# Kernel tuning notes

Measured on AMD Instinct MI355X. Metric: run time of the kernel, lower is better.

Reference implementation:

```python
import jax, jax.numpy as jnp
import numpy as np

N, E, D_IN, D_H, G = 50000, 800000, 300, 128, 128


def gat_conv(x, src, dst, W, att_src, att_dst, bias):
    # PyG GATConv, heads=1, concat, negative_slope=0.2, self-loops already appended.
    h = x @ W                              # [N, F]
    a_s = h @ att_src                      # [N]
    a_d = h @ att_dst                      # [N]
    e = jax.nn.leaky_relu(a_s[src] + a_d[dst], 0.2)   # [E+N]
    m = jax.ops.segment_max(e, dst, num_segments=h.shape[0])
    ex = jnp.exp(e - m[dst])
    denom = jax.ops.segment_sum(ex, dst, num_segments=h.shape[0])
    alpha = ex / denom[dst]                # softmax over in-edges of each dst
    out = jax.ops.segment_sum(alpha[:, None] * h[src], dst, num_segments=h.shape[0])
    return out + bias


def setup_inputs() -> dict:
    key = jax.random.key(0)
    ks = jax.random.split(key, 12)
    x = jax.random.normal(ks[0], (N, D_IN), dtype=jnp.float32)
    edge_index = jax.random.randint(ks[1], (2, E), 0, N)
    batch = jnp.sort(jax.random.randint(ks[2], (N,), 0, G))
    pos = jax.random.randint(ks[3], (N,), 0, 2).astype(bool)
    s = 0.05
    W1 = jax.random.normal(ks[4], (D_IN, D_H), dtype=jnp.float32) * s
    as1 = jax.random.normal(ks[5], (D_H,), dtype=jnp.float32) * s
    ad1 = jax.random.normal(ks[6], (D_H,), dtype=jnp.float32) * s
    b1 = jnp.zeros((D_H,), dtype=jnp.float32)
    W2 = jax.random.normal(ks[7], (D_H, D_H), dtype=jnp.float32) * s
    as2 = jax.random.normal(ks[8], (D_H,), dtype=jnp.float32) * s
    ad2 = jax.random.normal(ks[9], (D_H,), dtype=jnp.float32) * s
    b2 = jnp.zeros((D_H,), dtype=jnp.float32)
    Wfc = jax.random.normal(ks[10], (D_H, 1), dtype=jnp.float32) * s
    bfc = jnp.zeros((1,), dtype=jnp.float32)
    return {"x": x, "edge_index": edge_index, "batch": batch, "pos": pos,
            "num_graphs": G, "W1": W1, "as1": as1, "ad1": ad1, "b1": b1,
            "W2": W2, "as2": as2, "ad2": ad2, "b2": b2, "Wfc": Wfc, "bfc": bfc}


def reference(x, edge_index, batch, pos, num_graphs, W1, as1, ad1, b1,
              W2, as2, ad2, b2, Wfc, bfc):
    n = x.shape[0]
    loop = jnp.arange(n)
    src = jnp.concatenate([edge_index[0], loop])
    dst = jnp.concatenate([edge_index[1], loop])
    h = gat_conv(x, src, dst, W1, as1, ad1, b1)
    h = jax.nn.gelu(h, approximate=False)
    # dropout is identity in eval mode
    h = gat_conv(h, src, dst, W2, as2, ad2, b2)   # [N, 128]
    # masked per-graph mean: logits[g] = mean over nodes with batch==g and pos
    w = pos.astype(h.dtype)                       # [N]
    sums = jax.ops.segment_sum(h * w[:, None], batch, num_segments=num_graphs)
    cnt = jax.ops.segment_sum(w, batch, num_segments=num_graphs)
    logits = sums / jnp.maximum(cnt, 1.0)[:, None]          # [G, 128]
    scores = (jax.nn.gelu(logits, approximate=False) @ Wfc + bfc).reshape(-1, num_graphs)
    return scores, logits
```

## Files before the change

### kernel.cpp

```cpp
#include <hip/hip_runtime.h>
#include <math.h>

#define NN 50000
#define EE 800000
#define DIN 300
#define DH 128
#define NG 128
#define RSIZE 6250

typedef __attribute__((ext_vector_type(8))) short short8;
typedef __attribute__((ext_vector_type(4))) float floatx4;

__device__ __forceinline__ float gelu_exact(float x) {
  return 0.5f * x * (1.0f + erff(x * 0.7071067811865476f));
}

__device__ __forceinline__ void split_bf16(float v, unsigned short& hi, unsigned short& lo) {
  unsigned int u = __float_as_uint(v);
  hi = (unsigned short)(u >> 16);
  float fh = __uint_as_float((unsigned int)hi << 16);
  lo = (unsigned short)(__float_as_uint(v - fh) >> 16);
}

__device__ __forceinline__ unsigned short f2bf_rne(float x) {
  unsigned int u = __float_as_uint(x);
  unsigned int r = (u + 0x7FFFu + ((u >> 16) & 1u)) >> 16;
  return (unsigned short)r;
}

__device__ __forceinline__ float bf_lo(unsigned u) { return __uint_as_float(u << 16); }
__device__ __forceinline__ float bf_hi(unsigned u) { return __uint_as_float(u & 0xFFFF0000u); }

__device__ __forceinline__ void async_ld16(void* lds, const void* g) {
  __builtin_amdgcn_global_load_lds(
      (const __attribute__((address_space(1))) unsigned int*)(unsigned long long)g,
      (__attribute__((address_space(3))) unsigned int*)(unsigned int)(unsigned long long)lds,
      16, 0, 0);
}


__global__ __launch_bounds__(256) void count_part_kernel(const int* __restrict__ ei,
                                                         int* __restrict__ deg,
                                                         int blocksPerRange) {
  const int r = blockIdx.x & 7;
  const int t = blockIdx.x >> 3;
  const int lo = r * RSIZE, hi = lo + RSIZE;
  const int total = EE + NN;
  const int step = blocksPerRange * 256;
  for (int e0 = t * 256; e0 < total; e0 += step) {
    int e = e0 + threadIdx.x;
    if (e < total) {
      int d = (e < EE) ? ei[EE + e] : (e - EE);
      if (d >= lo && d < hi) atomicAdd(&deg[d], 1);
    }
  }
}

__global__ __launch_bounds__(1024) void scan_part_kernel(const int* __restrict__ deg,
                                                         int* __restrict__ rowptr,
                                                         int* __restrict__ bsum) {
  __shared__ int wsum[16];
  const int tid = threadIdx.x;
  const int lane = tid & 63;
  const int wid = tid >> 6;
  int idx = blockIdx.x * 1024 + tid;
  int v = (idx < NN) ? deg[idx] : 0;
  int x = v;
#pragma unroll
  for (int d = 1; d < 64; d <<= 1) {
    int y = __shfl_up(x, d, 64);
    if (lane >= d) x += y;
  }
  if (lane == 63) wsum[wid] = x;
  __syncthreads();
  if (wid == 0) {
    int s = (lane < 16) ? wsum[lane] : 0;
#pragma unroll
    for (int d = 1; d < 16; d <<= 1) {
      int y = __shfl_up(s, d, 64);
      if (lane >= d) s += y;
    }
    if (lane < 16) wsum[lane] = s;
  }
  __syncthreads();
  int woff = (wid > 0) ? wsum[wid - 1] : 0;
  int incl = x + woff;
  if (idx < NN) rowptr[idx] = incl - v;
  if (tid == 1023) bsum[blockIdx.x] = incl;
}

__global__ __launch_bounds__(64) void scan_sums_kernel(const int* __restrict__ bsum,
                                                       int* __restrict__ boff, int nb) {
  int lane = threadIdx.x;
  int v = (lane < nb) ? bsum[lane] : 0;
  int x = v;
#pragma unroll
  for (int d = 1; d < 64; d <<= 1) {
    int y = __shfl_up(x, d, 64);
    if (lane >= d) x += y;
  }
  if (lane < nb) boff[lane] = x - v;
  if (lane == nb - 1) boff[nb] = x;
}

__global__ __launch_bounds__(256) void scan_add_kernel(int* __restrict__ rowptr,
                                                       const int* __restrict__ boff,
                                                       int* __restrict__ cursor, int nb) {
  int i = blockIdx.x * 256 + threadIdx.x;
  if (i < NN) {
    int r = rowptr[i] + boff[i >> 10];
    rowptr[i] = r;
    cursor[i] = r;
  } else if (i == NN) {
    rowptr[NN] = boff[nb];
  }
}

__global__ __launch_bounds__(256) void scatter_part_kernel(const int* __restrict__ ei,
                                                           int* __restrict__ cursor,
                                                           int* __restrict__ colA,
                                                           int blocksPerRange) {
  const int r = blockIdx.x & 7;
  const int t = blockIdx.x >> 3;
  const int lo = r * RSIZE, hi = lo + RSIZE;
  const int total = EE + NN;
  const int step = blocksPerRange * 256;
  for (int e0 = t * 256; e0 < total; e0 += step) {
    int e = e0 + threadIdx.x;
    if (e < total) {
      int d = (e < EE) ? ei[EE + e] : (e - EE);
      if (d >= lo && d < hi) {
        int s = (e < EE) ? ei[e] : d;
        int p = atomicAdd(&cursor[d], 1);
        colA[p] = s;
      }
    }
  }
}


__global__ __launch_bounds__(256) void convert_bt_kernel(const float* __restrict__ B,
                                                         unsigned short* __restrict__ Bth,
                                                         unsigned short* __restrict__ Btl,
                                                         int K, int Kpad) {
  int i = blockIdx.x * 256 + threadIdx.x;
  int n = i / Kpad, k = i % Kpad;
  if (n >= 128) return;
  float v = (k < K) ? B[(long)k * 128 + n] : 0.f;
  unsigned short h, l;
  split_bf16(v, h, l);
  Bth[(long)n * Kpad + k] = h;
  Btl[(long)n * Kpad + k] = l;
}


__global__ __launch_bounds__(256) void gemm_mfma_kernel(
    const float* __restrict__ A,
    const unsigned short* __restrict__ Bth, const unsigned short* __restrict__ Btl,
    unsigned short* __restrict__ C, int M, int K, int Kpad,
    const float* __restrict__ avs, const float* __restrict__ avd,
    float* __restrict__ aS, float* __restrict__ aD) {
  __shared__ __align__(16) unsigned short Bls[2][2][128 * 32];

  const int tid = threadIdx.x;
  const int lane = tid & 63;
  const int w = tid >> 6;
  const int wr = w & 1;
  const int wc = w >> 1;
  const int q = lane >> 4;
  const int m16 = lane & 15;
  const int row0 = blockIdx.x * 32;
  const int myrow = row0 + wr * 16 + m16;
  const bool rok = myrow < M;
  const long abase = (long)myrow * K;

  const int rl = lane >> 2, qq0 = lane & 3;
  const int nb0 = w * 16 + rl;
  const int nb1 = 64 + w * 16 + rl;
  const long boff0 = (long)nb0 * Kpad + (long)((qq0 ^ ((nb0 >> 1) & 3)) * 8);
  const long boff1 = (long)nb1 * Kpad + (long)((qq0 ^ ((nb1 >> 1) & 3)) * 8);

  floatx4 acc[4];
#pragma unroll
  for (int i = 0; i < 4; i++) acc[i] = (floatx4)(0.f);

  const int nsteps = Kpad / 32;

  float4 vA0, vA1, nA0, nA1;
  nA0 = nA1 = make_float4(0.f, 0.f, 0.f, 0.f);

  auto stageB = [&](int s, int nb) {
    const int k0 = s * 32;
    async_ld16(&Bls[nb][0][(w * 16) * 32], Bth + boff0 + k0);
    async_ld16(&Bls[nb][0][(64 + w * 16) * 32], Bth + boff1 + k0);
    async_ld16(&Bls[nb][1][(w * 16) * 32], Btl + boff0 + k0);
    async_ld16(&Bls[nb][1][(64 + w * 16) * 32], Btl + boff1 + k0);
  };
  auto loadA = [&](int s, float4& x0, float4& x1) {
    const int k0 = s * 32 + q * 8;
    x0 = make_float4(0.f, 0.f, 0.f, 0.f);
    x1 = x0;
    if (rok) {
      if (k0 + 4 <= K) x0 = *(const float4*)&A[abase + k0];
      if (k0 + 8 <= K) x1 = *(const float4*)&A[abase + k0 + 4];
    }
  };

  stageB(0, 0);
  loadA(0, vA0, vA1);
  __syncthreads();

  for (int s = 0; s < nsteps; s++) {
    const int cur = s & 1;
    if (s + 1 < nsteps) {
      stageB(s + 1, 1 ^ cur);
      loadA(s + 1, nA0, nA1);
    }
    float av[8] = {vA0.x, vA0.y, vA0.z, vA0.w, vA1.x, vA1.y, vA1.z, vA1.w};
    union {
      unsigned u[4];
      short8 s8;
    } Uh, Ul;
#pragma unroll
    for (int i = 0; i < 4; i++) {
      unsigned short ha, la, hb, lb;
      split_bf16(av[2 * i], ha, la);
      split_bf16(av[2 * i + 1], hb, lb);
      Uh.u[i] = (unsigned)ha | ((unsigned)hb << 16);
      Ul.u[i] = (unsigned)la | ((unsigned)lb << 16);
    }
    short8 afh = Uh.s8, afl = Ul.s8;
#pragma unroll
    for (int ct = 0; ct < 4; ct++) {
      int n = wc * 64 + ct * 16 + m16;
      int qv = (q ^ ((n >> 1) & 3)) * 8;
      short8 bfh = *(const short8*)&Bls[cur][0][n * 32 + qv];
      short8 bfl = *(const short8*)&Bls[cur][1][n * 32 + qv];
      acc[ct] = __builtin_amdgcn_mfma_f32_16x16x32_bf16(afh, bfh, acc[ct], 0, 0, 0);
      acc[ct] = __builtin_amdgcn_mfma_f32_16x16x32_bf16(afh, bfl, acc[ct], 0, 0, 0);
      acc[ct] = __builtin_amdgcn_mfma_f32_16x16x32_bf16(afl, bfh, acc[ct], 0, 0, 0);
    }
    vA0 = nA0;
    vA1 = nA1;
    __syncthreads();
  }

  float avs_r[4], avd_r[4];
#pragma unroll
  for (int ct = 0; ct < 4; ct++) {
    avs_r[ct] = avs[wc * 64 + ct * 16 + m16];
    avd_r[ct] = avd[wc * 64 + ct * 16 + m16];
  }
  float psA[4], pdA[4];
#pragma unroll
  for (int reg = 0; reg < 4; reg++) {
    int grow = row0 + wr * 16 + q * 4 + reg;
    bool ok = grow < M;
    float ps = 0.f, pd = 0.f;
#pragma unroll
    for (int ct = 0; ct < 4; ct++) {
      float c = acc[ct][reg];
      if (ok) C[(long)grow * 128 + wc * 64 + ct * 16 + m16] = f2bf_rne(c);
      ps = fmaf(c, avs_r[ct], ps);
      pd = fmaf(c, avd_r[ct], pd);
    }
#pragma unroll
    for (int d = 1; d < 16; d <<= 1) {
      ps += __shfl_xor(ps, d, 64);
      pd += __shfl_xor(pd, d, 64);
    }
    psA[reg] = ps;
    pdA[reg] = pd;
  }
  float* redS = (float*)&Bls[0][0][0];
  float* redD = redS + 32;
  if (wc == 1 && m16 == 0) {
#pragma unroll
    for (int reg = 0; reg < 4; reg++) {
      int rloc = wr * 16 + q * 4 + reg;
      redS[rloc] = psA[reg];
      redD[rloc] = pdA[reg];
    }
  }
  __syncthreads();
  if (wc == 0 && m16 == 0) {
#pragma unroll
    for (int reg = 0; reg < 4; reg++) {
      int rloc = wr * 16 + q * 4 + reg;
      int grow = row0 + rloc;
      if (grow < M) {
        aS[grow] = psA[reg] + redS[rloc];
        aD[grow] = pdA[reg] + redD[rloc];
      }
    }
  }
}


__global__ __launch_bounds__(256) void aggregate_kernel(const int* __restrict__ rowptr,
                                                        const int* __restrict__ colA,
                                                        const float* __restrict__ aS,
                                                        const float* __restrict__ aD,
                                                        const unsigned short* __restrict__ Hb,
                                                        const float* __restrict__ bias,
                                                        float* __restrict__ out,
                                                        int apply_gelu) {
  const int lane = threadIdx.x & 63;
  const int dst = blockIdx.x * 4 + (threadIdx.x >> 6);
  if (dst >= NN) return;
  const int start = rowptr[dst];
  const int end = rowptr[dst + 1];
  const int deg = end - start;
  const float ad = aD[dst];
  const int half = lane >> 5;
  const int fl = lane & 31;

  float a0 = 0.f, a1 = 0.f, a2 = 0.f, a3 = 0.f;

  if (deg <= 64) {
    int src = 0;
    float e = -__builtin_inff();
    if (lane < deg) {
      src = colA[start + lane];
      float v = aS[src] + ad;
      e = (v > 0.f) ? v : 0.2f * v;
    }
    float mx = e;
#pragma unroll
    for (int d = 1; d < 64; d <<= 1) mx = fmaxf(mx, __shfl_xor(mx, d, 64));
    float ew = (lane < deg) ? expf(e - mx) : 0.f;
    float ss = ew;
#pragma unroll
    for (int d = 1; d < 64; d <<= 1) ss += __shfl_xor(ss, d, 64);
    float wgt = ew * (1.f / ss);
    for (int j = 0; j < deg; j += 8) {
      int sj[4];
      float wj[4];
#pragma unroll
      for (int i = 0; i < 4; i++) {
        int idx = j + 2 * i + half;
        sj[i] = __shfl(src, idx & 63, 64);
        float ww = __shfl(wgt, idx & 63, 64);
        wj[i] = (idx < deg) ? ww : 0.f;
      }
      uint2 u[4];
#pragma unroll
      for (int i = 0; i < 4; i++) u[i] = *(const uint2*)&Hb[(long)sj[i] * DH + fl * 4];
#pragma unroll
      for (int i = 0; i < 4; i++) {
        a0 = fmaf(wj[i], bf_lo(u[i].x), a0);
        a1 = fmaf(wj[i], bf_hi(u[i].x), a1);
        a2 = fmaf(wj[i], bf_lo(u[i].y), a2);
        a3 = fmaf(wj[i], bf_hi(u[i].y), a3);
      }
    }
  } else {
    float m = -__builtin_inff(), ssum = 0.f;
    for (int c0 = start; c0 < end; c0 += 64) {
      int i = c0 + lane;
      float e = -__builtin_inff();
      if (i < end) {
        int s = colA[i];
        float v = aS[s] + ad;
        e = (v > 0.f) ? v : 0.2f * v;
      }
      float cm = e;
#pragma unroll
      for (int d = 1; d < 64; d <<= 1) cm = fmaxf(cm, __shfl_xor(cm, d, 64));
      float ce = (i < end) ? expf(e - cm) : 0.f;
      float cs = ce;
#pragma unroll
      for (int d = 1; d < 64; d <<= 1) cs += __shfl_xor(cs, d, 64);
      float nm = fmaxf(m, cm);
      ssum = ssum * expf(m - nm) + cs * expf(cm - nm);
      m = nm;
    }
    float inv = 1.f / ssum;
    for (int c0 = start; c0 < end; c0 += 64) {
      int i = c0 + lane;
      int src = 0;
      float wgt = 0.f;
      if (i < end) {
        src = colA[i];
        float v = aS[src] + ad;
        float e = (v > 0.f) ? v : 0.2f * v;
        wgt = expf(e - m) * inv;
      }
      int lim = min(64, end - c0);
      for (int j = 0; j < lim; j += 4) {
        int j0 = j + half;
        int j1 = j + 2 + half;
        int sj0 = __shfl(src, j0 & 63, 64);
        float wj0 = __shfl(wgt, j0 & 63, 64);
        if (j0 >= lim) wj0 = 0.f;
        int sj1 = __shfl(src, j1 & 63, 64);
        float wj1 = __shfl(wgt, j1 & 63, 64);
        if (j1 >= lim) wj1 = 0.f;
        uint2 u0 = *(const uint2*)&Hb[(long)sj0 * DH + fl * 4];
        uint2 u1 = *(const uint2*)&Hb[(long)sj1 * DH + fl * 4];
        a0 = fmaf(wj0, bf_lo(u0.x), a0);
        a1 = fmaf(wj0, bf_hi(u0.x), a1);
        a2 = fmaf(wj0, bf_lo(u0.y), a2);
        a3 = fmaf(wj0, bf_hi(u0.y), a3);
        a0 = fmaf(wj1, bf_lo(u1.x), a0);
        a1 = fmaf(wj1, bf_hi(u1.x), a1);
        a2 = fmaf(wj1, bf_lo(u1.y), a2);
        a3 = fmaf(wj1, bf_hi(u1.y), a3);
      }
    }
  }

  a0 += __shfl_xor(a0, 32, 64);
  a1 += __shfl_xor(a1, 32, 64);
  a2 += __shfl_xor(a2, 32, 64);
  a3 += __shfl_xor(a3, 32, 64);

  if (half == 0) {
    float4 b = *(const float4*)&bias[fl * 4];
    float r0 = a0 + b.x;
    float r1 = a1 + b.y;
    float r2 = a2 + b.z;
    float r3 = a3 + b.w;
    if (apply_gelu) {
      r0 = gelu_exact(r0); r1 = gelu_exact(r1);
      r2 = gelu_exact(r2); r3 = gelu_exact(r3);
    }
    *(float4*)&out[(long)dst * DH + fl * 4] = make_float4(r0, r1, r2, r3);
  }
}


__global__ __launch_bounds__(128) void pool_kernel(const float* __restrict__ H,
                                                   const int* __restrict__ batch,
                                                   const int* __restrict__ pos,
                                                   float* __restrict__ sums,
                                                   float* __restrict__ cnt) {
  const int CH = 64;
  int n0 = blockIdx.x * CH;
  int n1 = min(n0 + CH, NN);
  int f = threadIdx.x;
  float acc = 0.f, c = 0.f;
  int g = batch[n0];
  for (int n = n0; n < n1; n++) {
    int gn = batch[n];
    if (gn != g) {
      atomicAdd(&sums[g * DH + f], acc);
      if (f == 0) atomicAdd(&cnt[g], c);
      acc = 0.f; c = 0.f; g = gn;
    }
    if (pos[n]) {
      acc += H[(long)n * DH + f];
      c += 1.f;
    }
  }
  atomicAdd(&sums[g * DH + f], acc);
  if (f == 0) atomicAdd(&cnt[g], c);
}


__global__ __launch_bounds__(128) void head_kernel(const float* __restrict__ sums,
                                                   const float* __restrict__ cnt,
                                                   const float* __restrict__ Wfc,
                                                   const float* __restrict__ bfc,
                                                   float* __restrict__ out) {
  int g = blockIdx.x;
  int f = threadIdx.x;
  float c = fmaxf(cnt[g], 1.f);
  float logit = sums[g * DH + f] / c;
  out[NG + g * DH + f] = logit;
  float gl = gelu_exact(logit) * Wfc[f];
  __shared__ float red[2];
#pragma unroll
  for (int d = 1; d < 64; d <<= 1) gl += __shfl_xor(gl, d, 64);
  int lane = f & 63, w = f >> 6;
  if (lane == 0) red[w] = gl;
  __syncthreads();
  if (f == 0) out[g] = red[0] + red[1] + bfc[0];
}


extern "C" void kernel_launch(void* const* d_in, const int* in_sizes, int n_in,
                              void* d_out, int out_size, void* d_ws, size_t ws_size,
                              hipStream_t stream) {
  const float* x   = (const float*)d_in[0];
  const int* ei    = (const int*)d_in[1];
  const int* batch = (const int*)d_in[2];
  const int* pos   = (const int*)d_in[3];
  const float* W1  = (const float*)d_in[5];
  const float* as1 = (const float*)d_in[6];
  const float* ad1 = (const float*)d_in[7];
  const float* b1  = (const float*)d_in[8];
  const float* W2  = (const float*)d_in[9];
  const float* as2 = (const float*)d_in[10];
  const float* ad2 = (const float*)d_in[11];
  const float* b2  = (const float*)d_in[12];
  const float* Wfc = (const float*)d_in[13];
  const float* bfc = (const float*)d_in[14];
  float* out = (float*)d_out;

  const int KP1 = 320;
  const int KP2 = 128;
  const int NB_SCAN = (NN + 1023) / 1024;
  const int BPR = 416;

  char* ws = (char*)d_ws;
  size_t off = 0;
  auto nxt = [&](size_t b) -> void* {
    size_t p = off;
    off += (b + 255) & ~(size_t)255;
    return (void*)(ws + p);
  };
  int* rowptr = (int*)nxt((NN + 1) * sizeof(int));
  int* cursor = (int*)nxt(NN * sizeof(int));
  int* colA   = (int*)nxt((size_t)(EE + NN) * sizeof(int));
  int* bsum   = (int*)nxt((NB_SCAN + 1) * sizeof(int));
  int* boff   = (int*)nxt((NB_SCAN + 1) * sizeof(int));
  float* aS   = (float*)nxt((size_t)2 * NN * sizeof(float));
  float* aD   = aS + NN;
  unsigned short* bufAb = (unsigned short*)nxt((size_t)NN * DH * sizeof(short));
  float* bufB = (float*)nxt((size_t)NN * DH * sizeof(float));
  float* sums = (float*)nxt((size_t)(NG * DH + NG) * sizeof(float));
  float* cnt  = sums + NG * DH;
  unsigned short* Bt1h = (unsigned short*)nxt((size_t)128 * KP1 * sizeof(short));
  unsigned short* Bt1l = (unsigned short*)nxt((size_t)128 * KP1 * sizeof(short));
  unsigned short* Bt2h = (unsigned short*)nxt((size_t)128 * KP2 * sizeof(short));
  unsigned short* Bt2l = (unsigned short*)nxt((size_t)128 * KP2 * sizeof(short));

  hipMemsetAsync(cursor, 0, NN * sizeof(int), stream);
  hipMemsetAsync(sums, 0, (NG * DH + NG) * sizeof(float), stream);

  convert_bt_kernel<<<(128 * KP1 + 255) / 256, 256, 0, stream>>>(W1, Bt1h, Bt1l, DIN, KP1);
  convert_bt_kernel<<<(128 * KP2 + 255) / 256, 256, 0, stream>>>(W2, Bt2h, Bt2l, DH, KP2);

  count_part_kernel<<<8 * BPR, 256, 0, stream>>>(ei, cursor, BPR);
  scan_part_kernel<<<NB_SCAN, 1024, 0, stream>>>(cursor, rowptr, bsum);
  scan_sums_kernel<<<1, 64, 0, stream>>>(bsum, boff, NB_SCAN);
  scan_add_kernel<<<(NN + 1 + 255) / 256, 256, 0, stream>>>(rowptr, boff, cursor, NB_SCAN);
  scatter_part_kernel<<<8 * BPR, 256, 0, stream>>>(ei, cursor, colA, BPR);

  const int gblocks = (NN + 31) / 32;
  gemm_mfma_kernel<<<gblocks, 256, 0, stream>>>(x, Bt1h, Bt1l, bufAb, NN, DIN, KP1,
                                                as1, ad1, aS, aD);
  aggregate_kernel<<<(NN + 3) / 4, 256, 0, stream>>>(rowptr, colA, aS, aD, bufAb, b1, bufB, 1);
  gemm_mfma_kernel<<<gblocks, 256, 0, stream>>>(bufB, Bt2h, Bt2l, bufAb, NN, DH, KP2,
                                                as2, ad2, aS, aD);
  aggregate_kernel<<<(NN + 3) / 4, 256, 0, stream>>>(rowptr, colA, aS, aD, bufAb, b2, bufB, 0);
  pool_kernel<<<(NN + 63) / 64, 128, 0, stream>>>(bufB, batch, pos, sums, cnt);
  head_kernel<<<NG, 128, 0, stream>>>(sums, cnt, Wfc, bfc, out);
}
```

Before: 348.4 us.

## Retile GEMM to 64x64 blocks over a 2D grid with atomic attention-score reduction

The GEMM block tile changes from 32 rows × 128 cols to 64 rows × 64 cols, with blockIdx.y choosing the column half. Each wave now owns 16 rows × 64 cols. This halves the shared B tile and removes the intra-block LDS reduction and barrier for the attention dot products. The per-row partial scores from the two column halves are now combined with float atomicAdd, which needs extra memsets of aS/aD before each GEMM. The trade-off is that each A row is read by two blocks instead of one, and the atomics make the summation order nondeterministic.

Result: no change. 355.0 us (+1.9%).

```diff
diff --git a/kernel.cpp b/kernel.cpp
--- a/kernel.cpp
+++ b/kernel.cpp
@@ -160,25 +160,22 @@
     unsigned short* __restrict__ C, int M, int K, int Kpad,
     const float* __restrict__ avs, const float* __restrict__ avd,
     float* __restrict__ aS, float* __restrict__ aD) {
-  __shared__ __align__(16) unsigned short Bls[2][2][128 * 32];
+  __shared__ __align__(16) unsigned short Bls[2][2][64 * 32];
 
   const int tid = threadIdx.x;
   const int lane = tid & 63;
   const int w = tid >> 6;
-  const int wr = w & 1;
-  const int wc = w >> 1;
   const int q = lane >> 4;
   const int m16 = lane & 15;
-  const int row0 = blockIdx.x * 32;
-  const int myrow = row0 + wr * 16 + m16;
+  const int row0 = blockIdx.x * 64 + w * 16;
+  const int col0 = blockIdx.y * 64;
+  const int myrow = row0 + m16;
   const bool rok = myrow < M;
   const long abase = (long)myrow * K;
 
   const int rl = lane >> 2, qq0 = lane & 3;
-  const int nb0 = w * 16 + rl;
-  const int nb1 = 64 + w * 16 + rl;
-  const long boff0 = (long)nb0 * Kpad + (long)((qq0 ^ ((nb0 >> 1) & 3)) * 8);
-  const long boff1 = (long)nb1 * Kpad + (long)((qq0 ^ ((nb1 >> 1) & 3)) * 8);
+  const int nl = w * 16 + rl;
+  const long boff = (long)(col0 + nl) * Kpad + (long)((qq0 ^ ((nl >> 1) & 3)) * 8);
 
   floatx4 acc[4];
 #pragma unroll
@@ -191,10 +188,8 @@
 
   auto stageB = [&](int s, int nb) {
     const int k0 = s * 32;
-    async_ld16(&Bls[nb][0][(w * 16) * 32], Bth + boff0 + k0);
-    async_ld16(&Bls[nb][0][(64 + w * 16) * 32], Bth + boff1 + k0);
-    async_ld16(&Bls[nb][1][(w * 16) * 32], Btl + boff0 + k0);
-    async_ld16(&Bls[nb][1][(64 + w * 16) * 32], Btl + boff1 + k0);
+    async_ld16(&Bls[nb][0][(w * 16) * 32], Bth + boff + k0);
+    async_ld16(&Bls[nb][1][(w * 16) * 32], Btl + boff + k0);
   };
   auto loadA = [&](int s, float4& x0, float4& x1) {
     const int k0 = s * 32 + q * 8;
@@ -232,7 +227,7 @@
     short8 afh = Uh.s8, afl = Ul.s8;
 #pragma unroll
     for (int ct = 0; ct < 4; ct++) {
-      int n = wc * 64 + ct * 16 + m16;
+      int n = ct * 16 + m16;
       int qv = (q ^ ((n >> 1) & 3)) * 8;
       short8 bfh = *(const short8*)&Bls[cur][0][n * 32 + qv];
       short8 bfl = *(const short8*)&Bls[cur][1][n * 32 + qv];
@@ -248,19 +243,18 @@
   float avs_r[4], avd_r[4];
 #pragma unroll
   for (int ct = 0; ct < 4; ct++) {
-    avs_r[ct] = avs[wc * 64 + ct * 16 + m16];
-    avd_r[ct] = avd[wc * 64 + ct * 16 + m16];
-  }
-  float psA[4], pdA[4];
+    avs_r[ct] = avs[col0 + ct * 16 + m16];
+    avd_r[ct] = avd[col0 + ct * 16 + m16];
+  }
 #pragma unroll
   for (int reg = 0; reg < 4; reg++) {
-    int grow = row0 + wr * 16 + q * 4 + reg;
+    int grow = row0 + q * 4 + reg;
     bool ok = grow < M;
     float ps = 0.f, pd = 0.f;
 #pragma unroll
     for (int ct = 0; ct < 4; ct++) {
       float c = acc[ct][reg];
-      if (ok) C[(long)grow * 128 + wc * 64 + ct * 16 + m16] = f2bf_rne(c);
+      if (ok) C[(long)grow * 128 + col0 + ct * 16 + m16] = f2bf_rne(c);
       ps = fmaf(c, avs_r[ct], ps);
       pd = fmaf(c, avd_r[ct], pd);
     }
@@ -269,29 +263,9 @@
       ps += __shfl_xor(ps, d, 64);
       pd += __shfl_xor(pd, d, 64);
     }
-    psA[reg] = ps;
-    pdA[reg] = pd;
-  }
-  float* redS = (float*)&Bls[0][0][0];
-  float* redD = redS + 32;
-  if (wc == 1 && m16 == 0) {
-#pragma unroll
-    for (int reg = 0; reg < 4; reg++) {
-      int rloc = wr * 16 + q * 4 + reg;
-      redS[rloc] = psA[reg];
-      redD[rloc] = pdA[reg];
-    }
-  }
-  __syncthreads();
-  if (wc == 0 && m16 == 0) {
-#pragma unroll
-    for (int reg = 0; reg < 4; reg++) {
-      int rloc = wr * 16 + q * 4 + reg;
-      int grow = row0 + rloc;
-      if (grow < M) {
-        aS[grow] = psA[reg] + redS[rloc];
-        aD[grow] = pdA[reg] + redD[rloc];
-      }
+    if (m16 == 0 && ok) {
+      atomicAdd(&aS[grow], ps);
+      atomicAdd(&aD[grow], pd);
     }
   }
 }
@@ -528,6 +502,7 @@
 
   hipMemsetAsync(cursor, 0, NN * sizeof(int), stream);
   hipMemsetAsync(sums, 0, (NG * DH + NG) * sizeof(float), stream);
+  hipMemsetAsync(aS, 0, (size_t)2 * NN * sizeof(float), stream);
 
   convert_bt_kernel<<<(128 * KP1 + 255) / 256, 256, 0, stream>>>(W1, Bt1h, Bt1l, DIN, KP1);
   convert_bt_kernel<<<(128 * KP2 + 255) / 256, 256, 0, stream>>>(W2, Bt2h, Bt2l, DH, KP2);
@@ -538,12 +513,13 @@
   scan_add_kernel<<<(NN + 1 + 255) / 256, 256, 0, stream>>>(rowptr, boff, cursor, NB_SCAN);
   scatter_part_kernel<<<8 * BPR, 256, 0, stream>>>(ei, cursor, colA, BPR);
 
-  const int gblocks = (NN + 31) / 32;
-  gemm_mfma_kernel<<<gblocks, 256, 0, stream>>>(x, Bt1h, Bt1l, bufAb, NN, DIN, KP1,
-                                                as1, ad1, aS, aD);
+  const dim3 ggrid((NN + 63) / 64, 2);
+  gemm_mfma_kernel<<<ggrid, 256, 0, stream>>>(x, Bt1h, Bt1l, bufAb, NN, DIN, KP1,
+                                              as1, ad1, aS, aD);
   aggregate_kernel<<<(NN + 3) / 4, 256, 0, stream>>>(rowptr, colA, aS, aD, bufAb, b1, bufB, 1);
-  gemm_mfma_kernel<<<gblocks, 256, 0, stream>>>(bufB, Bt2h, Bt2l, bufAb, NN, DH, KP2,
-                                                as2, ad2, aS, aD);
+  hipMemsetAsync(aS, 0, (size_t)2 * NN * sizeof(float), stream);
+  gemm_mfma_kernel<<<ggrid, 256, 0, stream>>>(bufB, Bt2h, Bt2l, bufAb, NN, DH, KP2,
+                                              as2, ad2, aS, aD);
   aggregate_kernel<<<(NN + 3) / 4, 256, 0, stream>>>(rowptr, colA, aS, aD, bufAb, b2, bufB, 0);
   pool_kernel<<<(NN + 63) / 64, 128, 0, stream>>>(bufB, batch, pos, sums, cnt);
   head_kernel<<<NG, 128, 0, stream>>>(sums, cnt, Wfc, bfc, out);
```
